# Kernel tuning notes

Measured on AMD Instinct MI355X. Metric: run time of the kernel, lower is better.

The kernel has to match this reference:

```python
import jax, jax.numpy as jnp
import numpy as np

H = 1024          # frame height (template.shape[0])
W = 1024          # frame width  (template.shape[1])
CD = 900          # center_dims
MS = 10           # ms_h = ms_w
EPS = 1e-8
CS = (H - CD) // 2        # c_shp_x = c_shp_y = 62
OFF = MS + CS             # template crop offset = 72
TW = H - 2 * OFF          # cropped template side = 880
S = 2 * MS + 1            # NCC map side = 21


def setup_inputs() -> dict:
    key = jax.random.key(0)
    k1, k2 = jax.random.split(key)
    # spatially-correlated synthetic frame so the NCC peak is real (log-peak interpolation valid)
    noise = jax.random.normal(k1, (1, H, W, 1), jnp.float32)
    smooth = jax.lax.reduce_window(noise, 0.0, jax.lax.add, (1, 15, 15, 1), (1, 1, 1, 1), 'SAME') / 225.0
    template = smooth[0, :, :, 0]
    X = jnp.roll(template, (3, -2), axis=(0, 1))[None, :, :, None] \
        + 0.05 * jax.random.normal(k2, (1, H, W, 1), jnp.float32)
    return {"X": X, "template": template}


def _forward(X, template):
    # --- template normalization (zero-mean, variance) ---
    tmpl = template[OFF:H - OFF, OFF:W - OFF]                  # (TW, TW)
    t_zm = tmpl - jnp.mean(tmpl)
    t_var = jnp.sum(t_zm * t_zm) + EPS                         # scalar

    # --- image local normalization over the template window ---
    Xc = X[:, CS:H - CS, CS:W - CS, :]                         # (1, CD, CD, 1)
    imgs_zm = Xc - jnp.mean(Xc, axis=(1, 2), keepdims=True)
    win = (1, TW, TW, 1)
    ls = jax.lax.reduce_window(Xc, 0.0, jax.lax.add, win, (1, 1, 1, 1), 'VALID')        # local sum  (1,S,S,1)
    lsq = jax.lax.reduce_window(Xc * Xc, 0.0, jax.lax.add, win, (1, 1, 1, 1), 'VALID')  # local sumsq
    var = lsq - ls * ls / (TW * TW) + EPS
    var = jnp.maximum(var, 0.0)

    # --- NCC numerator: correlate zero-mean image with zero-mean template ---
    num = jax.lax.conv_general_dilated(
        imgs_zm, t_zm[:, :, None, None], (1, 1), 'VALID',
        dimension_numbers=('NHWC', 'HWIO', 'NHWC'))           # (1, S, S, 1)
    ncc = num / jnp.sqrt(t_var * var)
    ncc = jnp.where(jnp.isnan(ncc), 0.0, ncc)

    # --- subpixel peak via log-Gaussian interpolation ---
    ncc2 = ncc[0, :, :, 0]                                     # (S, S)
    idx = jnp.argmax(ncc2.reshape(-1))
    sx = (idx // S).astype(jnp.int32)
    sy = (idx % S).astype(jnp.int32)
    lg = jnp.log(ncc2)

    def at(r, c):
        return lg[jnp.clip(r, 0, S - 1), jnp.clip(c, 0, S - 1)]

    l_xm1, l_xp1 = at(sx - 1, sy), at(sx + 1, sy)
    l_ym1, l_yp1 = at(sx, sy - 1), at(sx, sy + 1)
    l4 = 4.0 * at(sx, sy)
    xs = -(sx.astype(jnp.float32) - MS) - (l_xm1 - l_xp1) / (2 * l_xm1 - l4 + 2 * l_xp1)
    ys = -(sy.astype(jnp.float32) - MS) - (l_ym1 - l_yp1) / (2 * l_ym1 - l4 + 2 * l_yp1)

    # --- bilinear translate (tfa.image.translate semantics: out[r,c] = in[r-xs, c-ys], fill 0) ---
    img = X[0, :, :, 0]
    rr = jnp.arange(H, dtype=jnp.float32) - xs
    cc = jnp.arange(W, dtype=jnp.float32) - ys
    r0 = jnp.floor(rr)
    c0 = jnp.floor(cc)
    wr = (rr - r0)[:, None]
    wc = (cc - c0)[None, :]
    r0i = r0.astype(jnp.int32)
    c0i = c0.astype(jnp.int32)

    def samp(ri, ci):
        vr = ((ri >= 0) & (ri < H))[:, None]
        vc = ((ci >= 0) & (ci < W))[None, :]
        v = img[jnp.clip(ri, 0, H - 1)[:, None], jnp.clip(ci, 0, W - 1)[None, :]]
        return jnp.where(vr & vc, v, 0.0)

    out = ((1 - wr) * (1 - wc) * samp(r0i, c0i)
           + (1 - wr) * wc * samp(r0i, c0i + 1)
           + wr * (1 - wc) * samp(r0i + 1, c0i)
           + wr * wc * samp(r0i + 1, c0i + 1))                 # (H, W)

    flat = out.T.reshape(-1)[None, :]                          # matches reshape(transpose(squeeze(.)), [-1])[None,:]
    return flat, xs, ys


def reference(X, template):
    flat, xs, ys = _forward(X, template)
    return (flat, xs, ys)
```

## Files before the change

kernel.cpp:

```cpp
#include <hip/hip_runtime.h>
#include <math.h>

#define HH 1024
#define WW 1024
#define CD 900
#define MS 10
#define CS 62
#define OFFT 72
#define TW 880
#define SS 21
#define EPSV 1e-8
#define NBAND 55
#define RPB 16
#define NCH 55


__global__ __launch_bounds__(256) void row_stats_kernel(const float* __restrict__ X,
                                                        const float* __restrict__ T,
                                                        float* __restrict__ RS1T,
                                                        float* __restrict__ RS2T,
                                                        float* __restrict__ Trow1,
                                                        float* __restrict__ Trow2,
                                                        float* __restrict__ Sfull) {
    const int b = blockIdx.x, tid = threadIdx.x;
    __shared__ float red[4][3];
    const int lane = tid & 63, wid = tid >> 6;
    if (b < CD) {
        const float* row = X + (size_t)(CS + b) * WW + CS;
        float sf = 0.f, sw = 0.f, qw = 0.f;
        for (int v = tid; v < CD; v += 256) {
            float x = row[v];
            sf += x;
            if (v < TW) { sw += x; qw += x * x; }
        }
        for (int m = 1; m < 64; m <<= 1) {
            sf += __shfl_xor(sf, m); sw += __shfl_xor(sw, m); qw += __shfl_xor(qw, m);
        }
        if (lane == 0) { red[wid][0] = sf; red[wid][1] = sw; red[wid][2] = qw; }
        __syncthreads();
        if (tid < 32) {
            const float swb = red[0][1] + red[1][1] + red[2][1] + red[3][1];
            const float qwb = red[0][2] + red[1][2] + red[2][2] + red[3][2];
            float d1 = 0.f, d2 = 0.f;
            if (tid >= 1 && tid < SS) {
                float a = row[tid - 1], c2 = row[TW + tid - 1];
                d1 = c2 - a;
                d2 = c2 * c2 - a * a;
            }
            for (int off = 1; off < 32; off <<= 1) {
                float u1 = __shfl_up(d1, off), u2 = __shfl_up(d2, off);
                if (tid >= off) { d1 += u1; d2 += u2; }
            }
            if (tid < SS) {
                RS1T[tid * CD + b] = swb + d1;
                RS2T[tid * CD + b] = qwb + d2;
            }
            if (tid == 0) Sfull[b] = red[0][0] + red[1][0] + red[2][0] + red[3][0];
        }
    } else {
        const int u = b - CD;
        const float* row = T + (size_t)(OFFT + u) * WW + OFFT;
        float s = 0.f, q = 0.f;
        for (int v = tid; v < TW; v += 256) { float t = row[v]; s += t; q += t * t; }
        for (int m = 1; m < 64; m <<= 1) { s += __shfl_xor(s, m); q += __shfl_xor(q, m); }
        if (lane == 0) { red[wid][0] = s; red[wid][1] = q; }
        __syncthreads();
        if (tid == 0) {
            Trow1[u] = red[0][0] + red[1][0] + red[2][0] + red[3][0];
            Trow2[u] = red[0][1] + red[1][1] + red[2][1] + red[3][1];
        }
    }
}

__global__ __launch_bounds__(256) void corr_kernel(const float* __restrict__ X,
                                                   const float* __restrict__ T,
                                                   float* __restrict__ part) {
    const int band = blockIdx.x, i = blockIdx.y;
    const int tid = threadIdx.x;
    const int u0 = band * RPB;

    float acc[SS];
#pragma unroll
    for (int j = 0; j < SS; ++j) acc[j] = 0.f;

#pragma unroll 1
    for (int item = tid; item < RPB * NCH; item += 256) {
        const int ul = item / NCH;
        const int c = item - ul * NCH;
        const int u = u0 + ul;
        const float4* xp = (const float4*)(X + (size_t)(CS + i + u) * WW + 60 + c * 16);
        const float4* tp = (const float4*)(T + (size_t)(OFFT + u) * WW + OFFT + c * 16);
        float xr[40], t[16];
#pragma unroll
        for (int k = 0; k < 10; ++k) {
            float4 q = xp[k];
            xr[4 * k] = q.x; xr[4 * k + 1] = q.y; xr[4 * k + 2] = q.z; xr[4 * k + 3] = q.w;
        }
#pragma unroll
        for (int k = 0; k < 4; ++k) {
            float4 q = tp[k];
            t[4 * k] = q.x; t[4 * k + 1] = q.y; t[4 * k + 2] = q.z; t[4 * k + 3] = q.w;
        }
#pragma unroll
        for (int j = 0; j < SS; ++j) {
            float a = acc[j];
#pragma unroll
            for (int k = 0; k < 16; ++k) a = fmaf(xr[2 + j + k], t[k], a);
            acc[j] = a;
        }
    }

#pragma unroll
    for (int j = 0; j < SS; ++j)
#pragma unroll
        for (int m = 1; m < 64; m <<= 1) acc[j] += __shfl_xor(acc[j], m);

    __shared__ float red[4][SS];
    const int lane = tid & 63, wid = tid >> 6;
    if (lane == 0) {
#pragma unroll
        for (int j = 0; j < SS; ++j) red[wid][j] = acc[j];
    }
    __syncthreads();
    if (tid < SS) {
        float s = red[0][tid] + red[1][tid] + red[2][tid] + red[3][tid];
        part[(i * NBAND + band) * SS + tid] = s;
    }
}

__global__ __launch_bounds__(256) void ncc_final_kernel(const float* __restrict__ part,
                                                        const float* __restrict__ RS1T,
                                                        const float* __restrict__ RS2T,
                                                        const float* __restrict__ Trow1,
                                                        const float* __restrict__ Trow2,
                                                        const float* __restrict__ Sfull,
                                                        float* __restrict__ ncc) {
    const int bid = blockIdx.x;
    const int i = bid / SS, j = bid - i * SS;
    const int tid = threadIdx.x;
    double dd = 0, d1 = 0, d2 = 0, ta = 0, tb = 0, xs = 0;
    for (int b = tid; b < NBAND; b += 256) dd += (double)part[(i * NBAND + b) * SS + j];
    const float* r1 = RS1T + j * CD + i;
    const float* r2 = RS2T + j * CD + i;
    for (int u = tid; u < TW; u += 256) {
        d1 += (double)r1[u]; d2 += (double)r2[u];
        ta += (double)Trow1[u]; tb += (double)Trow2[u];
    }
    for (int k = tid; k < CD; k += 256) xs += (double)Sfull[k];
    for (int m = 1; m < 64; m <<= 1) {
        dd += __shfl_xor(dd, m); d1 += __shfl_xor(d1, m); d2 += __shfl_xor(d2, m);
        ta += __shfl_xor(ta, m); tb += __shfl_xor(tb, m); xs += __shfl_xor(xs, m);
    }
    __shared__ double red[4][6];
    const int lane = tid & 63, wid = tid >> 6;
    if (lane == 0) {
        red[wid][0] = dd; red[wid][1] = d1; red[wid][2] = d2;
        red[wid][3] = ta; red[wid][4] = tb; red[wid][5] = xs;
    }
    __syncthreads();
    if (tid == 0) {
        double dot = red[0][0] + red[1][0] + red[2][0] + red[3][0];
        double S1  = red[0][1] + red[1][1] + red[2][1] + red[3][1];
        double S2  = red[0][2] + red[1][2] + red[2][2] + red[3][2];
        double sum_t  = red[0][3] + red[1][3] + red[2][3] + red[3][3];
        double sum_t2 = red[0][4] + red[1][4] + red[2][4] + red[3][4];
        double sumX   = red[0][5] + red[1][5] + red[2][5] + red[3][5];
        const double NT = 774400.0;
        double mt = sum_t / NT, mx = sumX / 810000.0;
        double tvar = sum_t2 - sum_t * sum_t / NT + EPSV;
        double var = S2 - S1 * S1 / NT + EPSV;
        if (var < 0.0) var = 0.0;
        double cross = dot - mt * S1 - mx * sum_t + NT * mx * mt;
        float val = (float)(cross / sqrt(tvar * var));
        if (isnan(val)) val = 0.f;
        ncc[i * SS + j] = val;
    }
}

__global__ __launch_bounds__(256) void shift_kernel(const float* __restrict__ img,
                                                    const float* __restrict__ ncc,
                                                    float* __restrict__ out) {
    __shared__ float sv[256];
    __shared__ int si[256];
    __shared__ float sxy[2];
    __shared__ float tile[64][65];
    const int tid = threadIdx.x;

    {
        float v = -1e30f; int vi = 0;
        for (int k = tid; k < SS * SS; k += 256) {
            float q = ncc[k];
            if (q > v) { v = q; vi = k; }
        }
        sv[tid] = v; si[tid] = vi;
        __syncthreads();
        for (int off = 128; off > 0; off >>= 1) {
            if (tid < off) {
                float v2 = sv[tid + off]; int i2 = si[tid + off];
                if (v2 > sv[tid] || (v2 == sv[tid] && i2 < si[tid])) { sv[tid] = v2; si[tid] = i2; }
            }
            __syncthreads();
        }
        if (tid == 0) {
            int idx = si[0];
            int sx = idx / SS;
            int sy = idx - sx * SS;
            auto at = [&](int r, int c) -> float {
                r = r < 0 ? 0 : (r > SS - 1 ? SS - 1 : r);
                c = c < 0 ? 0 : (c > SS - 1 ? SS - 1 : c);
                return logf(ncc[r * SS + c]);
            };
            float l4 = 4.0f * at(sx, sy);
            float lxm = at(sx - 1, sy), lxp = at(sx + 1, sy);
            float lym = at(sx, sy - 1), lyp = at(sx, sy + 1);
            float xsv = -((float)sx - (float)MS) - (lxm - lxp) / (2.0f * lxm - l4 + 2.0f * lxp);
            float ysv = -((float)sy - (float)MS) - (lym - lyp) / (2.0f * lym - l4 + 2.0f * lyp);
            sxy[0] = xsv; sxy[1] = ysv;
            if (blockIdx.x == 0 && blockIdx.y == 0) {
                out[(size_t)HH * WW] = xsv;
                out[(size_t)HH * WW + 1] = ysv;
            }
        }
        __syncthreads();
    }

    const float xs = sxy[0], ys = sxy[1];
    const int R0 = blockIdx.y * 64, C0 = blockIdx.x * 64;
    {
        const int cl = tid & 63, rg = tid >> 6;
        const int c = C0 + cl;
        const float cc = (float)c - ys;
        const float c0f = floorf(cc);
        const float wc = cc - c0f;
        const int c0 = (int)c0f;
        const bool vc0 = (c0 >= 0) & (c0 < WW);
        const bool vc1 = (c0 + 1 >= 0) & (c0 + 1 < WW);
        const int c0c = c0 < 0 ? 0 : (c0 > WW - 1 ? WW - 1 : c0);
        const int c1c = (c0 + 1) < 0 ? 0 : ((c0 + 1) > WW - 1 ? WW - 1 : c0 + 1);
        for (int k = 0; k < 16; ++k) {
            const int rl = rg * 16 + k;
            const int r = R0 + rl;
            const float rr = (float)r - xs;
            const float r0f = floorf(rr);
            const float wr = rr - r0f;
            const int r0 = (int)r0f;
            const bool vr0 = (r0 >= 0) & (r0 < HH);
            const bool vr1 = (r0 + 1 >= 0) & (r0 + 1 < HH);
            const int r0c = r0 < 0 ? 0 : (r0 > HH - 1 ? HH - 1 : r0);
            const int r1c = (r0 + 1) < 0 ? 0 : ((r0 + 1) > HH - 1 ? HH - 1 : r0 + 1);
            float s00 = img[(size_t)r0c * WW + c0c]; if (!(vr0 & vc0)) s00 = 0.f;
            float s01 = img[(size_t)r0c * WW + c1c]; if (!(vr0 & vc1)) s01 = 0.f;
            float s10 = img[(size_t)r1c * WW + c0c]; if (!(vr1 & vc0)) s10 = 0.f;
            float s11 = img[(size_t)r1c * WW + c1c]; if (!(vr1 & vc1)) s11 = 0.f;
            tile[rl][cl] = (1.f - wr) * (1.f - wc) * s00 + (1.f - wr) * wc * s01 +
                           wr * (1.f - wc) * s10 + wr * wc * s11;
        }
    }
    __syncthreads();
    {
        const int rl = tid & 63, cg = tid >> 6;
        for (int k = 0; k < 16; ++k) {
            const int cl = cg * 16 + k;
            out[(size_t)(C0 + cl) * HH + R0 + rl] = tile[rl][cl];
        }
    }
}

extern "C" void kernel_launch(void* const* d_in, const int* in_sizes, int n_in,
                              void* d_out, int out_size, void* d_ws, size_t ws_size,
                              hipStream_t stream) {
    const float* X = (const float*)d_in[0];
    const float* T = (const float*)d_in[1];
    float* out = (float*)d_out;

    char* w = (char*)d_ws;
    float* RS1T  = (float*)(w + 0);
    float* RS2T  = (float*)(w + 75600);
    float* Trow1 = (float*)(w + 151200);
    float* Trow2 = (float*)(w + 154720);
    float* Sfull = (float*)(w + 158240);
    float* part  = (float*)(w + 161840);
    float* ncc   = (float*)(w + 258880);

    row_stats_kernel<<<CD + TW, 256, 0, stream>>>(X, T, RS1T, RS2T, Trow1, Trow2, Sfull);
    corr_kernel<<<dim3(NBAND, SS), 256, 0, stream>>>(X, T, part);
    ncc_final_kernel<<<SS * SS, 256, 0, stream>>>(part, RS1T, RS2T, Trow1, Trow2, Sfull, ncc);
    shift_kernel<<<dim3(16, 16), 256, 0, stream>>>(X, ncc, out);
}
```

Before: 100.9 us.

## Fuse four kernels into one persistent cooperative kernel with grid syncs

Merges the row-stats, correlation, NCC-finalize and shift kernels into a single cooperative persistent kernel. Phases are separated by grid.sync() and blocks loop over virtual block indices, which removes three kernel launches and their gaps. The shift phase now uses 32x32 tiles, and every block redundantly recomputes the argmax and subpixel peak. In exchange it adds grid-sync cost and occupancy limits from the cooperative launch, and the grid size is derived from an occupancy query with a hard-coded 256 CU count.

```diff
diff --git a/kernel.cpp b/kernel.cpp
--- a/kernel.cpp
+++ b/kernel.cpp
@@ -1,5 +1,8 @@
 #include <hip/hip_runtime.h>
+#include <hip/hip_cooperative_groups.h>
 #include <math.h>
+
+namespace cg = cooperative_groups;
 
 #define HH 1024
 #define WW 1024
@@ -13,178 +16,188 @@
 #define NBAND 55
 #define RPB 16
 #define NCH 55
-
-
-__global__ __launch_bounds__(256) void row_stats_kernel(const float* __restrict__ X,
-                                                        const float* __restrict__ T,
-                                                        float* __restrict__ RS1T,
-                                                        float* __restrict__ RS2T,
-                                                        float* __restrict__ Trow1,
-                                                        float* __restrict__ Trow2,
-                                                        float* __restrict__ Sfull) {
-    const int b = blockIdx.x, tid = threadIdx.x;
-    __shared__ float red[4][3];
+#define NCORR (SS * NBAND)
+#define NSTAT (CD + TW)
+#define TOTAL_A (NCORR + NSTAT)
+
+#define O_RS1T 0
+#define O_RS2T 18900
+#define O_TROW1 37800
+#define O_TROW2 38680
+#define O_SFULL 39560
+#define O_PART 40460
+#define O_NCC 64715
+
+union SharedU {
+    float redf[4][SS];
+    double redd[4][6];
+    struct {
+        float sv[256];
+        int si[256];
+        float sxy[2];
+        float tile[32][33];
+    } c;
+};
+
+__global__ __launch_bounds__(256, 4) void fused_kernel(const float* __restrict__ X,
+                                                       const float* __restrict__ T,
+                                                       float* __restrict__ ws,
+                                                       float* __restrict__ out) {
+    float* RS1T = ws + O_RS1T;
+    float* RS2T = ws + O_RS2T;
+    float* Trow1 = ws + O_TROW1;
+    float* Trow2 = ws + O_TROW2;
+    float* Sfull = ws + O_SFULL;
+    float* part = ws + O_PART;
+    float* ncc = ws + O_NCC;
+
+    __shared__ SharedU su;
+    const int tid = threadIdx.x;
     const int lane = tid & 63, wid = tid >> 6;
-    if (b < CD) {
-        const float* row = X + (size_t)(CS + b) * WW + CS;
-        float sf = 0.f, sw = 0.f, qw = 0.f;
-        for (int v = tid; v < CD; v += 256) {
-            float x = row[v];
-            sf += x;
-            if (v < TW) { sw += x; qw += x * x; }
-        }
+    cg::grid_group grid = cg::this_grid();
+
+    for (int vb = blockIdx.x; vb < TOTAL_A; vb += gridDim.x) {
+        if (vb < NCORR) {
+            const int i = vb / NBAND;
+            const int band = vb - i * NBAND;
+            const int u0 = band * RPB;
+            float acc[SS];
+#pragma unroll
+            for (int j = 0; j < SS; ++j) acc[j] = 0.f;
+#pragma unroll 1
+            for (int item = tid; item < RPB * NCH; item += 256) {
+                const int ul = item / NCH;
+                const int c = item - ul * NCH;
+                const int u = u0 + ul;
+                const float4* xp = (const float4*)(X + (size_t)(CS + i + u) * WW + 60 + c * 16);
+                const float4* tp = (const float4*)(T + (size_t)(OFFT + u) * WW + OFFT + c * 16);
+                float xr[40], t[16];
+#pragma unroll
+                for (int k = 0; k < 10; ++k) {
+                    float4 q = xp[k];
+                    xr[4 * k] = q.x; xr[4 * k + 1] = q.y; xr[4 * k + 2] = q.z; xr[4 * k + 3] = q.w;
+                }
+#pragma unroll
+                for (int k = 0; k < 4; ++k) {
+                    float4 q = tp[k];
+                    t[4 * k] = q.x; t[4 * k + 1] = q.y; t[4 * k + 2] = q.z; t[4 * k + 3] = q.w;
+                }
+#pragma unroll
+                for (int j = 0; j < SS; ++j) {
+                    float a = acc[j];
+#pragma unroll
+                    for (int k = 0; k < 16; ++k) a = fmaf(xr[2 + j + k], t[k], a);
+                    acc[j] = a;
+                }
+            }
+#pragma unroll
+            for (int j = 0; j < SS; ++j)
+#pragma unroll
+                for (int m = 1; m < 64; m <<= 1) acc[j] += __shfl_xor(acc[j], m);
+            if (lane == 0) {
+#pragma unroll
+                for (int j = 0; j < SS; ++j) su.redf[wid][j] = acc[j];
+            }
+            __syncthreads();
+            if (tid < SS) {
+                float s = su.redf[0][tid] + su.redf[1][tid] + su.redf[2][tid] + su.redf[3][tid];
+                part[(i * NBAND + band) * SS + tid] = s;
+            }
+        } else {
+            const int b = vb - NCORR;
+            if (b < CD) {
+                const float* row = X + (size_t)(CS + b) * WW + CS;
+                float sf = 0.f, sw = 0.f, qw = 0.f;
+                for (int v = tid; v < CD; v += 256) {
+                    float x = row[v];
+                    sf += x;
+                    if (v < TW) { sw += x; qw += x * x; }
+                }
+                for (int m = 1; m < 64; m <<= 1) {
+                    sf += __shfl_xor(sf, m); sw += __shfl_xor(sw, m); qw += __shfl_xor(qw, m);
+                }
+                if (lane == 0) { su.redf[wid][0] = sf; su.redf[wid][1] = sw; su.redf[wid][2] = qw; }
+                __syncthreads();
+                if (tid < 32) {
+                    const float swb = su.redf[0][1] + su.redf[1][1] + su.redf[2][1] + su.redf[3][1];
+                    const float qwb = su.redf[0][2] + su.redf[1][2] + su.redf[2][2] + su.redf[3][2];
+                    float d1 = 0.f, d2 = 0.f;
+                    if (tid >= 1 && tid < SS) {
+                        float a = row[tid - 1], c2 = row[TW + tid - 1];
+                        d1 = c2 - a;
+                        d2 = c2 * c2 - a * a;
+                    }
+                    for (int off = 1; off < 32; off <<= 1) {
+                        float u1 = __shfl_up(d1, off), u2 = __shfl_up(d2, off);
+                        if (tid >= off) { d1 += u1; d2 += u2; }
+                    }
+                    if (tid < SS) {
+                        RS1T[tid * CD + b] = swb + d1;
+                        RS2T[tid * CD + b] = qwb + d2;
+                    }
+                    if (tid == 0)
+                        Sfull[b] = su.redf[0][0] + su.redf[1][0] + su.redf[2][0] + su.redf[3][0];
+                }
+            } else {
+                const int u = b - CD;
+                const float* row = T + (size_t)(OFFT + u) * WW + OFFT;
+                float s = 0.f, q = 0.f;
+                for (int v = tid; v < TW; v += 256) { float t = row[v]; s += t; q += t * t; }
+                for (int m = 1; m < 64; m <<= 1) { s += __shfl_xor(s, m); q += __shfl_xor(q, m); }
+                if (lane == 0) { su.redf[wid][0] = s; su.redf[wid][1] = q; }
+                __syncthreads();
+                if (tid == 0) {
+                    Trow1[u] = su.redf[0][0] + su.redf[1][0] + su.redf[2][0] + su.redf[3][0];
+                    Trow2[u] = su.redf[0][1] + su.redf[1][1] + su.redf[2][1] + su.redf[3][1];
+                }
+            }
+        }
+        __syncthreads();
+    }
+
+    grid.sync();
+
+    for (int vb = blockIdx.x; vb < SS * SS; vb += gridDim.x) {
+        const int i = vb / SS, j = vb - i * SS;
+        double dd = 0, d1 = 0, d2 = 0, ta = 0, tb = 0, xs = 0;
+        for (int b = tid; b < NBAND; b += 256) dd += (double)part[(i * NBAND + b) * SS + j];
+        const float* r1 = RS1T + j * CD + i;
+        const float* r2 = RS2T + j * CD + i;
+        for (int u = tid; u < TW; u += 256) {
+            d1 += (double)r1[u]; d2 += (double)r2[u];
+            ta += (double)Trow1[u]; tb += (double)Trow2[u];
+        }
+        for (int k = tid; k < CD; k += 256) xs += (double)Sfull[k];
         for (int m = 1; m < 64; m <<= 1) {
-            sf += __shfl_xor(sf, m); sw += __shfl_xor(sw, m); qw += __shfl_xor(qw, m);
-        }
-        if (lane == 0) { red[wid][0] = sf; red[wid][1] = sw; red[wid][2] = qw; }
-        __syncthreads();
-        if (tid < 32) {
-            const float swb = red[0][1] + red[1][1] + red[2][1] + red[3][1];
-            const float qwb = red[0][2] + red[1][2] + red[2][2] + red[3][2];
-            float d1 = 0.f, d2 = 0.f;
-            if (tid >= 1 && tid < SS) {
-                float a = row[tid - 1], c2 = row[TW + tid - 1];
-                d1 = c2 - a;
-                d2 = c2 * c2 - a * a;
-            }
-            for (int off = 1; off < 32; off <<= 1) {
-                float u1 = __shfl_up(d1, off), u2 = __shfl_up(d2, off);
-                if (tid >= off) { d1 += u1; d2 += u2; }
-            }
-            if (tid < SS) {
-                RS1T[tid * CD + b] = swb + d1;
-                RS2T[tid * CD + b] = qwb + d2;
-            }
-            if (tid == 0) Sfull[b] = red[0][0] + red[1][0] + red[2][0] + red[3][0];
-        }
-    } else {
-        const int u = b - CD;
-        const float* row = T + (size_t)(OFFT + u) * WW + OFFT;
-        float s = 0.f, q = 0.f;
-        for (int v = tid; v < TW; v += 256) { float t = row[v]; s += t; q += t * t; }
-        for (int m = 1; m < 64; m <<= 1) { s += __shfl_xor(s, m); q += __shfl_xor(q, m); }
-        if (lane == 0) { red[wid][0] = s; red[wid][1] = q; }
+            dd += __shfl_xor(dd, m); d1 += __shfl_xor(d1, m); d2 += __shfl_xor(d2, m);
+            ta += __shfl_xor(ta, m); tb += __shfl_xor(tb, m); xs += __shfl_xor(xs, m);
+        }
+        if (lane == 0) {
+            su.redd[wid][0] = dd; su.redd[wid][1] = d1; su.redd[wid][2] = d2;
+            su.redd[wid][3] = ta; su.redd[wid][4] = tb; su.redd[wid][5] = xs;
+        }
         __syncthreads();
         if (tid == 0) {
-            Trow1[u] = red[0][0] + red[1][0] + red[2][0] + red[3][0];
-            Trow2[u] = red[0][1] + red[1][1] + red[2][1] + red[3][1];
-        }
+            double dot = su.redd[0][0] + su.redd[1][0] + su.redd[2][0] + su.redd[3][0];
+            double S1 = su.redd[0][1] + su.redd[1][1] + su.redd[2][1] + su.redd[3][1];
+            double S2 = su.redd[0][2] + su.redd[1][2] + su.redd[2][2] + su.redd[3][2];
+            double sum_t = su.redd[0][3] + su.redd[1][3] + su.redd[2][3] + su.redd[3][3];
+            double sum_t2 = su.redd[0][4] + su.redd[1][4] + su.redd[2][4] + su.redd[3][4];
+            double sumX = su.redd[0][5] + su.redd[1][5] + su.redd[2][5] + su.redd[3][5];
+            const double NT = 774400.0;
+            double mt = sum_t / NT, mx = sumX / 810000.0;
+            double tvar = sum_t2 - sum_t * sum_t / NT + EPSV;
+            double var = S2 - S1 * S1 / NT + EPSV;
+            if (var < 0.0) var = 0.0;
+            double cross = dot - mt * S1 - mx * sum_t + NT * mx * mt;
+            float val = (float)(cross / sqrt(tvar * var));
+            if (isnan(val)) val = 0.f;
+            ncc[i * SS + j] = val;
+        }
+        __syncthreads();
     }
-}
-
-__global__ __launch_bounds__(256) void corr_kernel(const float* __restrict__ X,
-                                                   const float* __restrict__ T,
-                                                   float* __restrict__ part) {
-    const int band = blockIdx.x, i = blockIdx.y;
-    const int tid = threadIdx.x;
-    const int u0 = band * RPB;
-
-    float acc[SS];
-#pragma unroll
-    for (int j = 0; j < SS; ++j) acc[j] = 0.f;
-
-#pragma unroll 1
-    for (int item = tid; item < RPB * NCH; item += 256) {
-        const int ul = item / NCH;
-        const int c = item - ul * NCH;
-        const int u = u0 + ul;
-        const float4* xp = (const float4*)(X + (size_t)(CS + i + u) * WW + 60 + c * 16);
-        const float4* tp = (const float4*)(T + (size_t)(OFFT + u) * WW + OFFT + c * 16);
-        float xr[40], t[16];
-#pragma unroll
-        for (int k = 0; k < 10; ++k) {
-            float4 q = xp[k];
-            xr[4 * k] = q.x; xr[4 * k + 1] = q.y; xr[4 * k + 2] = q.z; xr[4 * k + 3] = q.w;
-        }
-#pragma unroll
-        for (int k = 0; k < 4; ++k) {
-            float4 q = tp[k];
-            t[4 * k] = q.x; t[4 * k + 1] = q.y; t[4 * k + 2] = q.z; t[4 * k + 3] = q.w;
-        }
-#pragma unroll
-        for (int j = 0; j < SS; ++j) {
-            float a = acc[j];
-#pragma unroll
-            for (int k = 0; k < 16; ++k) a = fmaf(xr[2 + j + k], t[k], a);
-            acc[j] = a;
-        }
-    }
-
-#pragma unroll
-    for (int j = 0; j < SS; ++j)
-#pragma unroll
-        for (int m = 1; m < 64; m <<= 1) acc[j] += __shfl_xor(acc[j], m);
-
-    __shared__ float red[4][SS];
-    const int lane = tid & 63, wid = tid >> 6;
-    if (lane == 0) {
-#pragma unroll
-        for (int j = 0; j < SS; ++j) red[wid][j] = acc[j];
-    }
-    __syncthreads();
-    if (tid < SS) {
-        float s = red[0][tid] + red[1][tid] + red[2][tid] + red[3][tid];
-        part[(i * NBAND + band) * SS + tid] = s;
-    }
-}
-
-__global__ __launch_bounds__(256) void ncc_final_kernel(const float* __restrict__ part,
-                                                        const float* __restrict__ RS1T,
-                                                        const float* __restrict__ RS2T,
-                                                        const float* __restrict__ Trow1,
-                                                        const float* __restrict__ Trow2,
-                                                        const float* __restrict__ Sfull,
-                                                        float* __restrict__ ncc) {
-    const int bid = blockIdx.x;
-    const int i = bid / SS, j = bid - i * SS;
-    const int tid = threadIdx.x;
-    double dd = 0, d1 = 0, d2 = 0, ta = 0, tb = 0, xs = 0;
-    for (int b = tid; b < NBAND; b += 256) dd += (double)part[(i * NBAND + b) * SS + j];
-    const float* r1 = RS1T + j * CD + i;
-    const float* r2 = RS2T + j * CD + i;
-    for (int u = tid; u < TW; u += 256) {
-        d1 += (double)r1[u]; d2 += (double)r2[u];
-        ta += (double)Trow1[u]; tb += (double)Trow2[u];
-    }
-    for (int k = tid; k < CD; k += 256) xs += (double)Sfull[k];
-    for (int m = 1; m < 64; m <<= 1) {
-        dd += __shfl_xor(dd, m); d1 += __shfl_xor(d1, m); d2 += __shfl_xor(d2, m);
-        ta += __shfl_xor(ta, m); tb += __shfl_xor(tb, m); xs += __shfl_xor(xs, m);
-    }
-    __shared__ double red[4][6];
-    const int lane = tid & 63, wid = tid >> 6;
-    if (lane == 0) {
-        red[wid][0] = dd; red[wid][1] = d1; red[wid][2] = d2;
-        red[wid][3] = ta; red[wid][4] = tb; red[wid][5] = xs;
-    }
-    __syncthreads();
-    if (tid == 0) {
-        double dot = red[0][0] + red[1][0] + red[2][0] + red[3][0];
-        double S1  = red[0][1] + red[1][1] + red[2][1] + red[3][1];
-        double S2  = red[0][2] + red[1][2] + red[2][2] + red[3][2];
-        double sum_t  = red[0][3] + red[1][3] + red[2][3] + red[3][3];
-        double sum_t2 = red[0][4] + red[1][4] + red[2][4] + red[3][4];
-        double sumX   = red[0][5] + red[1][5] + red[2][5] + red[3][5];
-        const double NT = 774400.0;
-        double mt = sum_t / NT, mx = sumX / 810000.0;
-        double tvar = sum_t2 - sum_t * sum_t / NT + EPSV;
-        double var = S2 - S1 * S1 / NT + EPSV;
-        if (var < 0.0) var = 0.0;
-        double cross = dot - mt * S1 - mx * sum_t + NT * mx * mt;
-        float val = (float)(cross / sqrt(tvar * var));
-        if (isnan(val)) val = 0.f;
-        ncc[i * SS + j] = val;
-    }
-}
-
-__global__ __launch_bounds__(256) void shift_kernel(const float* __restrict__ img,
-                                                    const float* __restrict__ ncc,
-                                                    float* __restrict__ out) {
-    __shared__ float sv[256];
-    __shared__ int si[256];
-    __shared__ float sxy[2];
-    __shared__ float tile[64][65];
-    const int tid = threadIdx.x;
+
+    grid.sync();
 
     {
         float v = -1e30f; int vi = 0;
@@ -192,17 +205,19 @@
             float q = ncc[k];
             if (q > v) { v = q; vi = k; }
         }
-        sv[tid] = v; si[tid] = vi;
+        su.c.sv[tid] = v; su.c.si[tid] = vi;
         __syncthreads();
         for (int off = 128; off > 0; off >>= 1) {
             if (tid < off) {
-                float v2 = sv[tid + off]; int i2 = si[tid + off];
-                if (v2 > sv[tid] || (v2 == sv[tid] && i2 < si[tid])) { sv[tid] = v2; si[tid] = i2; }
+                float v2 = su.c.sv[tid + off]; int i2 = su.c.si[tid + off];
+                if (v2 > su.c.sv[tid] || (v2 == su.c.sv[tid] && i2 < su.c.si[tid])) {
+                    su.c.sv[tid] = v2; su.c.si[tid] = i2;
+                }
             }
             __syncthreads();
         }
         if (tid == 0) {
-            int idx = si[0];
+            int idx = su.c.si[0];
             int sx = idx / SS;
             int sy = idx - sx * SS;
             auto at = [&](int r, int c) -> float {
@@ -215,54 +230,60 @@
             float lym = at(sx, sy - 1), lyp = at(sx, sy + 1);
             float xsv = -((float)sx - (float)MS) - (lxm - lxp) / (2.0f * lxm - l4 + 2.0f * lxp);
             float ysv = -((float)sy - (float)MS) - (lym - lyp) / (2.0f * lym - l4 + 2.0f * lyp);
-            sxy[0] = xsv; sxy[1] = ysv;
-            if (blockIdx.x == 0 && blockIdx.y == 0) {
+            su.c.sxy[0] = xsv; su.c.sxy[1] = ysv;
+            if (blockIdx.x == 0) {
                 out[(size_t)HH * WW] = xsv;
                 out[(size_t)HH * WW + 1] = ysv;
             }
         }
         __syncthreads();
     }
-
-    const float xs = sxy[0], ys = sxy[1];
-    const int R0 = blockIdx.y * 64, C0 = blockIdx.x * 64;
-    {
-        const int cl = tid & 63, rg = tid >> 6;
-        const int c = C0 + cl;
-        const float cc = (float)c - ys;
-        const float c0f = floorf(cc);
-        const float wc = cc - c0f;
-        const int c0 = (int)c0f;
-        const bool vc0 = (c0 >= 0) & (c0 < WW);
-        const bool vc1 = (c0 + 1 >= 0) & (c0 + 1 < WW);
-        const int c0c = c0 < 0 ? 0 : (c0 > WW - 1 ? WW - 1 : c0);
-        const int c1c = (c0 + 1) < 0 ? 0 : ((c0 + 1) > WW - 1 ? WW - 1 : c0 + 1);
-        for (int k = 0; k < 16; ++k) {
-            const int rl = rg * 16 + k;
-            const int r = R0 + rl;
-            const float rr = (float)r - xs;
-            const float r0f = floorf(rr);
-            const float wr = rr - r0f;
-            const int r0 = (int)r0f;
-            const bool vr0 = (r0 >= 0) & (r0 < HH);
-            const bool vr1 = (r0 + 1 >= 0) & (r0 + 1 < HH);
-            const int r0c = r0 < 0 ? 0 : (r0 > HH - 1 ? HH - 1 : r0);
-            const int r1c = (r0 + 1) < 0 ? 0 : ((r0 + 1) > HH - 1 ? HH - 1 : r0 + 1);
-            float s00 = img[(size_t)r0c * WW + c0c]; if (!(vr0 & vc0)) s00 = 0.f;
-            float s01 = img[(size_t)r0c * WW + c1c]; if (!(vr0 & vc1)) s01 = 0.f;
-            float s10 = img[(size_t)r1c * WW + c0c]; if (!(vr1 & vc0)) s10 = 0.f;
-            float s11 = img[(size_t)r1c * WW + c1c]; if (!(vr1 & vc1)) s11 = 0.f;
-            tile[rl][cl] = (1.f - wr) * (1.f - wc) * s00 + (1.f - wr) * wc * s01 +
-                           wr * (1.f - wc) * s10 + wr * wc * s11;
-        }
-    }
-    __syncthreads();
-    {
-        const int rl = tid & 63, cg = tid >> 6;
-        for (int k = 0; k < 16; ++k) {
-            const int cl = cg * 16 + k;
-            out[(size_t)(C0 + cl) * HH + R0 + rl] = tile[rl][cl];
-        }
+    const float xs = su.c.sxy[0], ys = su.c.sxy[1];
+
+    for (int vt = blockIdx.x; vt < 1024; vt += gridDim.x) {
+        const int bx = vt & 31, by = vt >> 5;
+        const int R0 = by * 32, C0 = bx * 32;
+        {
+            const int cl = tid & 31, rg = tid >> 5;
+            const int c = C0 + cl;
+            const float cc = (float)c - ys;
+            const float c0f = floorf(cc);
+            const float wc = cc - c0f;
+            const int c0 = (int)c0f;
+            const bool vc0 = (c0 >= 0) & (c0 < WW);
+            const bool vc1 = (c0 + 1 >= 0) & (c0 + 1 < WW);
+            const int c0c = c0 < 0 ? 0 : (c0 > WW - 1 ? WW - 1 : c0);
+            const int c1c = (c0 + 1) < 0 ? 0 : ((c0 + 1) > WW - 1 ? WW - 1 : c0 + 1);
+#pragma unroll
+            for (int k = 0; k < 4; ++k) {
+                const int rl = rg * 4 + k;
+                const int r = R0 + rl;
+                const float rr = (float)r - xs;
+                const float r0f = floorf(rr);
+                const float wr = rr - r0f;
+                const int r0 = (int)r0f;
+                const bool vr0 = (r0 >= 0) & (r0 < HH);
+                const bool vr1 = (r0 + 1 >= 0) & (r0 + 1 < HH);
+                const int r0c = r0 < 0 ? 0 : (r0 > HH - 1 ? HH - 1 : r0);
+                const int r1c = (r0 + 1) < 0 ? 0 : ((r0 + 1) > HH - 1 ? HH - 1 : r0 + 1);
+                float s00 = X[(size_t)r0c * WW + c0c]; if (!(vr0 & vc0)) s00 = 0.f;
+                float s01 = X[(size_t)r0c * WW + c1c]; if (!(vr0 & vc1)) s01 = 0.f;
+                float s10 = X[(size_t)r1c * WW + c0c]; if (!(vr1 & vc0)) s10 = 0.f;
+                float s11 = X[(size_t)r1c * WW + c1c]; if (!(vr1 & vc1)) s11 = 0.f;
+                su.c.tile[rl][cl] = (1.f - wr) * (1.f - wc) * s00 + (1.f - wr) * wc * s01 +
+                                    wr * (1.f - wc) * s10 + wr * wc * s11;
+            }
+        }
+        __syncthreads();
+        {
+            const int rl = tid & 31, cg2 = tid >> 5;
+#pragma unroll
+            for (int k = 0; k < 4; ++k) {
+                const int cl = cg2 * 4 + k;
+                out[(size_t)(C0 + cl) * HH + R0 + rl] = su.c.tile[rl][cl];
+            }
+        }
+        __syncthreads();
     }
 }
 
@@ -272,18 +293,14 @@
     const float* X = (const float*)d_in[0];
     const float* T = (const float*)d_in[1];
     float* out = (float*)d_out;
-
-    char* w = (char*)d_ws;
-    float* RS1T  = (float*)(w + 0);
-    float* RS2T  = (float*)(w + 75600);
-    float* Trow1 = (float*)(w + 151200);
-    float* Trow2 = (float*)(w + 154720);
-    float* Sfull = (float*)(w + 158240);
-    float* part  = (float*)(w + 161840);
-    float* ncc   = (float*)(w + 258880);
-
-    row_stats_kernel<<<CD + TW, 256, 0, stream>>>(X, T, RS1T, RS2T, Trow1, Trow2, Sfull);
-    corr_kernel<<<dim3(NBAND, SS), 256, 0, stream>>>(X, T, part);
-    ncc_final_kernel<<<SS * SS, 256, 0, stream>>>(part, RS1T, RS2T, Trow1, Trow2, Sfull, ncc);
-    shift_kernel<<<dim3(16, 16), 256, 0, stream>>>(X, ncc, out);
+    float* ws = (float*)d_ws;
+
+    int nb = 0;
+    hipError_t e = hipOccupancyMaxActiveBlocksPerMultiprocessor(&nb, fused_kernel, 256, 0);
+    if (e != hipSuccess || nb < 1) nb = 2;
+    int grid = nb * 256;
+    if (grid > 1024) grid = 1024;
+
+    void* args[] = {(void*)&X, (void*)&T, (void*)&ws, (void*)&out};
+    hipLaunchCooperativeKernel(fused_kernel, dim3(grid), dim3(256), args, 0, stream);
 }
```

New measurement: 223.9 us. 2.22x slower.

## Fuse row-stats and correlation kernels into one launch with double-buffered loads

Applied to the files above, without the earlier changes.

Merges the row statistics kernel and the correlation kernel into a single grid, where the first blocks compute correlation partials and the remaining blocks compute row and template statistics. This removes one launch and lets the two independent workloads run concurrently. The correlation loop is manually unrolled into four items with A/B register buffers so the next item's loads are issued before the current FMAs. A launch_bounds occupancy hint of 3 is added. The cost is higher register pressure from holding two item buffers.

```diff
diff --git a/kernel.cpp b/kernel.cpp
--- a/kernel.cpp
+++ b/kernel.cpp
@@ -13,128 +13,157 @@
 #define NBAND 55
 #define RPB 16
 #define NCH 55
-
-
-__global__ __launch_bounds__(256) void row_stats_kernel(const float* __restrict__ X,
-                                                        const float* __restrict__ T,
-                                                        float* __restrict__ RS1T,
-                                                        float* __restrict__ RS2T,
-                                                        float* __restrict__ Trow1,
-                                                        float* __restrict__ Trow2,
-                                                        float* __restrict__ Sfull) {
-    const int b = blockIdx.x, tid = threadIdx.x;
-    __shared__ float red[4][3];
+#define NITEMS (RPB * NCH)
+#define NCORR (SS * NBAND)
+#define NSTAT (CD + TW)
+
+#define O_RS1T 0
+#define O_RS2T 18900
+#define O_TROW1 37800
+#define O_TROW2 38680
+#define O_SFULL 39560
+#define O_PART 40460
+#define O_NCC 64715
+
+#define LOAD_ITEM(XR, TT, ITEM)                                                      \
+    {                                                                                \
+        const int ul_ = (ITEM) / NCH;                                                \
+        const int c_ = (ITEM) - ul_ * NCH;                                           \
+        const int u_ = u0 + ul_;                                                     \
+        const float4* xp_ = (const float4*)(X + (size_t)(CS + i + u_) * WW + 60 + c_ * 16); \
+        const float4* tp_ = (const float4*)(T + (size_t)(OFFT + u_) * WW + OFFT + c_ * 16); \
+        _Pragma("unroll") for (int k_ = 0; k_ < 10; ++k_) {                          \
+            float4 q_ = xp_[k_];                                                     \
+            XR[4 * k_] = q_.x; XR[4 * k_ + 1] = q_.y;                                \
+            XR[4 * k_ + 2] = q_.z; XR[4 * k_ + 3] = q_.w;                            \
+        }                                                                            \
+        _Pragma("unroll") for (int k_ = 0; k_ < 4; ++k_) {                           \
+            float4 q_ = tp_[k_];                                                     \
+            TT[4 * k_] = q_.x; TT[4 * k_ + 1] = q_.y;                                \
+            TT[4 * k_ + 2] = q_.z; TT[4 * k_ + 3] = q_.w;                            \
+        }                                                                            \
+    }
+
+#define FMA_ITEM(XR, TT)                                                             \
+    {                                                                                \
+        _Pragma("unroll") for (int j_ = 0; j_ < SS; ++j_) {                          \
+            float a_ = acc[j_];                                                      \
+            _Pragma("unroll") for (int k_ = 0; k_ < 16; ++k_)                        \
+                a_ = fmaf(XR[2 + j_ + k_], TT[k_], a_);                              \
+            acc[j_] = a_;                                                            \
+        }                                                                            \
+    }
+
+__global__ __launch_bounds__(256, 3) void corr_stats_kernel(const float* __restrict__ X,
+                                                            const float* __restrict__ T,
+                                                            float* __restrict__ ws) {
+    float* RS1T = ws + O_RS1T;
+    float* RS2T = ws + O_RS2T;
+    float* Trow1 = ws + O_TROW1;
+    float* Trow2 = ws + O_TROW2;
+    float* Sfull = ws + O_SFULL;
+    float* part = ws + O_PART;
+
+    const int tid = threadIdx.x;
     const int lane = tid & 63, wid = tid >> 6;
-    if (b < CD) {
-        const float* row = X + (size_t)(CS + b) * WW + CS;
-        float sf = 0.f, sw = 0.f, qw = 0.f;
-        for (int v = tid; v < CD; v += 256) {
-            float x = row[v];
-            sf += x;
-            if (v < TW) { sw += x; qw += x * x; }
-        }
-        for (int m = 1; m < 64; m <<= 1) {
-            sf += __shfl_xor(sf, m); sw += __shfl_xor(sw, m); qw += __shfl_xor(qw, m);
-        }
-        if (lane == 0) { red[wid][0] = sf; red[wid][1] = sw; red[wid][2] = qw; }
+    __shared__ float red[4][SS];
+
+    if (blockIdx.x < NCORR) {
+        const int vb = blockIdx.x;
+        const int i = vb / NBAND;
+        const int band = vb - i * NBAND;
+        const int u0 = band * RPB;
+
+        float acc[SS];
+#pragma unroll
+        for (int j = 0; j < SS; ++j) acc[j] = 0.f;
+
+        float xrA[40], ttA[16], xrB[40], ttB[16];
+        LOAD_ITEM(xrA, ttA, tid)
+        LOAD_ITEM(xrB, ttB, tid + 256)
+        FMA_ITEM(xrA, ttA)
+        LOAD_ITEM(xrA, ttA, tid + 512)
+        FMA_ITEM(xrB, ttB)
+        if (tid < NITEMS - 768) {
+            LOAD_ITEM(xrB, ttB, tid + 768)
+        }
+        FMA_ITEM(xrA, ttA)
+        if (tid < NITEMS - 768) {
+            FMA_ITEM(xrB, ttB)
+        }
+
+#pragma unroll
+        for (int j = 0; j < SS; ++j)
+#pragma unroll
+            for (int m = 1; m < 64; m <<= 1) acc[j] += __shfl_xor(acc[j], m);
+        if (lane == 0) {
+#pragma unroll
+            for (int j = 0; j < SS; ++j) red[wid][j] = acc[j];
+        }
         __syncthreads();
-        if (tid < 32) {
-            const float swb = red[0][1] + red[1][1] + red[2][1] + red[3][1];
-            const float qwb = red[0][2] + red[1][2] + red[2][2] + red[3][2];
-            float d1 = 0.f, d2 = 0.f;
-            if (tid >= 1 && tid < SS) {
-                float a = row[tid - 1], c2 = row[TW + tid - 1];
-                d1 = c2 - a;
-                d2 = c2 * c2 - a * a;
-            }
-            for (int off = 1; off < 32; off <<= 1) {
-                float u1 = __shfl_up(d1, off), u2 = __shfl_up(d2, off);
-                if (tid >= off) { d1 += u1; d2 += u2; }
-            }
-            if (tid < SS) {
-                RS1T[tid * CD + b] = swb + d1;
-                RS2T[tid * CD + b] = qwb + d2;
-            }
-            if (tid == 0) Sfull[b] = red[0][0] + red[1][0] + red[2][0] + red[3][0];
+        if (tid < SS) {
+            float s = red[0][tid] + red[1][tid] + red[2][tid] + red[3][tid];
+            part[(i * NBAND + band) * SS + tid] = s;
         }
     } else {
-        const int u = b - CD;
-        const float* row = T + (size_t)(OFFT + u) * WW + OFFT;
-        float s = 0.f, q = 0.f;
-        for (int v = tid; v < TW; v += 256) { float t = row[v]; s += t; q += t * t; }
-        for (int m = 1; m < 64; m <<= 1) { s += __shfl_xor(s, m); q += __shfl_xor(q, m); }
-        if (lane == 0) { red[wid][0] = s; red[wid][1] = q; }
-        __syncthreads();
-        if (tid == 0) {
-            Trow1[u] = red[0][0] + red[1][0] + red[2][0] + red[3][0];
-            Trow2[u] = red[0][1] + red[1][1] + red[2][1] + red[3][1];
+        const int b = blockIdx.x - NCORR;
+        if (b < CD) {
+            const float* row = X + (size_t)(CS + b) * WW + CS;
+            float sf = 0.f, sw = 0.f, qw = 0.f;
+            for (int v = tid; v < CD; v += 256) {
+                float x = row[v];
+                sf += x;
+                if (v < TW) { sw += x; qw += x * x; }
+            }
+            for (int m = 1; m < 64; m <<= 1) {
+                sf += __shfl_xor(sf, m); sw += __shfl_xor(sw, m); qw += __shfl_xor(qw, m);
+            }
+            if (lane == 0) { red[wid][0] = sf; red[wid][1] = sw; red[wid][2] = qw; }
+            __syncthreads();
+            if (tid < 32) {
+                const float swb = red[0][1] + red[1][1] + red[2][1] + red[3][1];
+                const float qwb = red[0][2] + red[1][2] + red[2][2] + red[3][2];
+                float d1 = 0.f, d2 = 0.f;
+                if (tid >= 1 && tid < SS) {
+                    float a = row[tid - 1], c2 = row[TW + tid - 1];
+                    d1 = c2 - a;
+                    d2 = c2 * c2 - a * a;
+                }
+                for (int off = 1; off < 32; off <<= 1) {
+                    float u1 = __shfl_up(d1, off), u2 = __shfl_up(d2, off);
+                    if (tid >= off) { d1 += u1; d2 += u2; }
+                }
+                if (tid < SS) {
+                    RS1T[tid * CD + b] = swb + d1;
+                    RS2T[tid * CD + b] = qwb + d2;
+                }
+                if (tid == 0) Sfull[b] = red[0][0] + red[1][0] + red[2][0] + red[3][0];
+            }
+        } else {
+            const int u = b - CD;
+            const float* row = T + (size_t)(OFFT + u) * WW + OFFT;
+            float s = 0.f, q = 0.f;
+            for (int v = tid; v < TW; v += 256) { float t = row[v]; s += t; q += t * t; }
+            for (int m = 1; m < 64; m <<= 1) { s += __shfl_xor(s, m); q += __shfl_xor(q, m); }
+            if (lane == 0) { red[wid][0] = s; red[wid][1] = q; }
+            __syncthreads();
+            if (tid == 0) {
+                Trow1[u] = red[0][0] + red[1][0] + red[2][0] + red[3][0];
+                Trow2[u] = red[0][1] + red[1][1] + red[2][1] + red[3][1];
+            }
         }
     }
 }
 
-__global__ __launch_bounds__(256) void corr_kernel(const float* __restrict__ X,
-                                                   const float* __restrict__ T,
-                                                   float* __restrict__ part) {
-    const int band = blockIdx.x, i = blockIdx.y;
-    const int tid = threadIdx.x;
-    const int u0 = band * RPB;
-
-    float acc[SS];
-#pragma unroll
-    for (int j = 0; j < SS; ++j) acc[j] = 0.f;
-
-#pragma unroll 1
-    for (int item = tid; item < RPB * NCH; item += 256) {
-        const int ul = item / NCH;
-        const int c = item - ul * NCH;
-        const int u = u0 + ul;
-        const float4* xp = (const float4*)(X + (size_t)(CS + i + u) * WW + 60 + c * 16);
-        const float4* tp = (const float4*)(T + (size_t)(OFFT + u) * WW + OFFT + c * 16);
-        float xr[40], t[16];
-#pragma unroll
-        for (int k = 0; k < 10; ++k) {
-            float4 q = xp[k];
-            xr[4 * k] = q.x; xr[4 * k + 1] = q.y; xr[4 * k + 2] = q.z; xr[4 * k + 3] = q.w;
-        }
-#pragma unroll
-        for (int k = 0; k < 4; ++k) {
-            float4 q = tp[k];
-            t[4 * k] = q.x; t[4 * k + 1] = q.y; t[4 * k + 2] = q.z; t[4 * k + 3] = q.w;
-        }
-#pragma unroll
-        for (int j = 0; j < SS; ++j) {
-            float a = acc[j];
-#pragma unroll
-            for (int k = 0; k < 16; ++k) a = fmaf(xr[2 + j + k], t[k], a);
-            acc[j] = a;
-        }
-    }
-
-#pragma unroll
-    for (int j = 0; j < SS; ++j)
-#pragma unroll
-        for (int m = 1; m < 64; m <<= 1) acc[j] += __shfl_xor(acc[j], m);
-
-    __shared__ float red[4][SS];
-    const int lane = tid & 63, wid = tid >> 6;
-    if (lane == 0) {
-#pragma unroll
-        for (int j = 0; j < SS; ++j) red[wid][j] = acc[j];
-    }
-    __syncthreads();
-    if (tid < SS) {
-        float s = red[0][tid] + red[1][tid] + red[2][tid] + red[3][tid];
-        part[(i * NBAND + band) * SS + tid] = s;
-    }
-}
-
-__global__ __launch_bounds__(256) void ncc_final_kernel(const float* __restrict__ part,
-                                                        const float* __restrict__ RS1T,
-                                                        const float* __restrict__ RS2T,
-                                                        const float* __restrict__ Trow1,
-                                                        const float* __restrict__ Trow2,
-                                                        const float* __restrict__ Sfull,
+__global__ __launch_bounds__(256) void ncc_final_kernel(const float* __restrict__ ws,
                                                         float* __restrict__ ncc) {
+    const float* RS1T = ws + O_RS1T;
+    const float* RS2T = ws + O_RS2T;
+    const float* Trow1 = ws + O_TROW1;
+    const float* Trow2 = ws + O_TROW2;
+    const float* Sfull = ws + O_SFULL;
+    const float* part = ws + O_PART;
+
     const int bid = blockIdx.x;
     const int i = bid / SS, j = bid - i * SS;
     const int tid = threadIdx.x;
@@ -160,11 +189,11 @@
     __syncthreads();
     if (tid == 0) {
         double dot = red[0][0] + red[1][0] + red[2][0] + red[3][0];
-        double S1  = red[0][1] + red[1][1] + red[2][1] + red[3][1];
-        double S2  = red[0][2] + red[1][2] + red[2][2] + red[3][2];
-        double sum_t  = red[0][3] + red[1][3] + red[2][3] + red[3][3];
+        double S1 = red[0][1] + red[1][1] + red[2][1] + red[3][1];
+        double S2 = red[0][2] + red[1][2] + red[2][2] + red[3][2];
+        double sum_t = red[0][3] + red[1][3] + red[2][3] + red[3][3];
         double sum_t2 = red[0][4] + red[1][4] + red[2][4] + red[3][4];
-        double sumX   = red[0][5] + red[1][5] + red[2][5] + red[3][5];
+        double sumX = red[0][5] + red[1][5] + red[2][5] + red[3][5];
         const double NT = 774400.0;
         double mt = sum_t / NT, mx = sumX / 810000.0;
         double tvar = sum_t2 - sum_t * sum_t / NT + EPSV;
@@ -272,18 +301,10 @@
     const float* X = (const float*)d_in[0];
     const float* T = (const float*)d_in[1];
     float* out = (float*)d_out;
-
-    char* w = (char*)d_ws;
-    float* RS1T  = (float*)(w + 0);
-    float* RS2T  = (float*)(w + 75600);
-    float* Trow1 = (float*)(w + 151200);
-    float* Trow2 = (float*)(w + 154720);
-    float* Sfull = (float*)(w + 158240);
-    float* part  = (float*)(w + 161840);
-    float* ncc   = (float*)(w + 258880);
-
-    row_stats_kernel<<<CD + TW, 256, 0, stream>>>(X, T, RS1T, RS2T, Trow1, Trow2, Sfull);
-    corr_kernel<<<dim3(NBAND, SS), 256, 0, stream>>>(X, T, part);
-    ncc_final_kernel<<<SS * SS, 256, 0, stream>>>(part, RS1T, RS2T, Trow1, Trow2, Sfull, ncc);
+    float* ws = (float*)d_ws;
+    float* ncc = ws + O_NCC;
+
+    corr_stats_kernel<<<NCORR + NSTAT, 256, 0, stream>>>(X, T, ws);
+    ncc_final_kernel<<<SS * SS, 256, 0, stream>>>(ws, ncc);
     shift_kernel<<<dim3(16, 16), 256, 0, stream>>>(X, ncc, out);
 }
```

Result: slower. 146.7 us (+45.4%).
